# Kernel tuning notes

Hardware: AMD Instinct MI355X
Metric: run time of the kernel (lower is better)

The kernel has to match this reference:

```python
import jax, jax.numpy as jnp
import numpy as np

N = 100000
E = 1600000
F_IN = 128
F_OUT = 128


def setup_inputs() -> dict:
    key = jax.random.key(0)
    k1, k2, k3, k4 = jax.random.split(key, 4)
    x = jax.random.normal(k1, (N, F_IN), dtype=jnp.float32)
    edge_index = jax.random.randint(k2, (2, E), 0, N, dtype=jnp.int64)
    # GCNConv params (glorot weight, zero bias as in PyG defaults)
    limit = float(np.sqrt(6.0 / (F_IN + F_OUT)))
    W = jax.random.uniform(k3, (F_IN, F_OUT), minval=-limit, maxval=limit, dtype=jnp.float32)
    b = jnp.zeros((F_OUT,), dtype=jnp.float32)
    return {"x": x, "edge_index": edge_index, "W": W, "b": b}


def reference(x, edge_index, W, b):
    n = x.shape[0]
    # add self-loops
    loops = jnp.arange(n, dtype=edge_index.dtype)
    src = jnp.concatenate([edge_index[0], loops])  # source nodes j
    dst = jnp.concatenate([edge_index[1], loops])  # target nodes i
    # symmetric normalization: deg over incoming edges (targets), weight 1
    deg = jax.ops.segment_sum(jnp.ones_like(dst, dtype=x.dtype), dst, num_segments=n)
    dinv = jnp.where(deg > 0, jax.lax.rsqrt(deg), 0.0)
    norm = dinv[src] * dinv[dst]  # [E+N]
    # linear transform then message passing
    h = x @ W  # [N, F_OUT]
    msgs = h[src] * norm[:, None]  # gather + scale, [E+N, F_OUT]
    out = jax.ops.segment_sum(msgs, dst, num_segments=n)  # scatter-add
    return out + b
```

## Files before the change

kernel.cpp:

```cpp
#include <hip/hip_runtime.h>

#define FDIM 128
#define NBMAX 512
#define EPB 4096
#define CPAD 16

typedef __attribute__((ext_vector_type(8))) short bf16x8;
typedef __attribute__((ext_vector_type(4))) float f32x4;

__device__ __forceinline__ unsigned short f2bf(float f) {
    unsigned int u = __float_as_uint(f);
    unsigned int r = u + 0x7fffu + ((u >> 16) & 1u);
    return (unsigned short)(r >> 16);
}

__global__ __launch_bounds__(256) void k_prep(const int* __restrict__ dst,
                                              int* __restrict__ bcnt,
                                              const float* __restrict__ W,
                                              unsigned short* __restrict__ whi,
                                              int e, int ebl) {
    __shared__ int h[NBMAX];
    if ((int)blockIdx.x < ebl) {
        for (int i = threadIdx.x; i < NBMAX; i += 256) h[i] = 0;
        __syncthreads();
        int base = blockIdx.x * EPB;
        int end = min(base + EPB, e);
        for (int i = base + threadIdx.x; i < end; i += 256) atomicAdd(&h[dst[i] >> 8], 1);
        __syncthreads();
        for (int i = threadIdx.x; i < NBMAX; i += 256) {
            int c = h[i];
            if (c) atomicAdd(&bcnt[i * CPAD], c);
        }
    } else {
        int id = ((int)blockIdx.x - ebl) * 256 + threadIdx.x;
        int k = id >> 7, nn = id & 127;
        whi[nn * FDIM + k] = f2bf(W[id]);
    }
}

__global__ __launch_bounds__(256) void k_main(
    const int* __restrict__ src, const int* __restrict__ dst,
    const int* __restrict__ bcnt,
    int* __restrict__ gcur,
    unsigned int* __restrict__ coarse,
    const float* __restrict__ x, const unsigned short* __restrict__ whi,
    unsigned short* __restrict__ hs, int e, int n, int ebl) {
    union ShU {
        unsigned short Bs[FDIM * FDIM];
        struct {
            int sval[EPB];
            unsigned short sbkt[EPB];
            int loff[NBMAX];
            int gbs[NBMAX];
        } sc;
    };
    __shared__ ShU S;
    __shared__ int cur[NBMAX];
    __shared__ int bb[NBMAX];

    if ((int)blockIdx.x < ebl) {
        const int t = threadIdx.x;
        int* scr = S.sc.sval;

        int v0 = bcnt[t * CPAD], v1 = bcnt[(t + 256) * CPAD];
        scr[t] = v0;
        scr[t + 256] = v1;
        __syncthreads();
        for (int off = 1; off < NBMAX; off <<= 1) {
            int a0 = (t >= off) ? scr[t - off] : 0;
            int a1 = (t + 256 >= off) ? scr[t + 256 - off] : 0;
            __syncthreads();
            scr[t] += a0;
            scr[t + 256] += a1;
            __syncthreads();
        }
        bb[t] = scr[t] - v0;
        bb[t + 256] = scr[t + 256] - v1;

        cur[t] = 0;
        cur[t + 256] = 0;
        __syncthreads();
        int base = blockIdx.x * EPB;
        int end = min(base + EPB, e);
        int cnt = end - base;
        for (int i = base + t; i < end; i += 256) atomicAdd(&cur[dst[i] >> 8], 1);
        __syncthreads();

        int c0 = cur[t], c1 = cur[t + 256];
        scr[t] = c0;
        scr[t + 256] = c1;
        __syncthreads();
        for (int off = 1; off < NBMAX; off <<= 1) {
            int a0 = (t >= off) ? scr[t - off] : 0;
            int a1 = (t + 256 >= off) ? scr[t + 256 - off] : 0;
            __syncthreads();
            scr[t] += a0;
            scr[t + 256] += a1;
            __syncthreads();
        }
        S.sc.loff[t] = scr[t] - c0;
        S.sc.loff[t + 256] = scr[t + 256] - c1;
        S.sc.gbs[t] = bb[t] + (c0 ? atomicAdd(&gcur[t * CPAD], c0) : 0);
        S.sc.gbs[t + 256] = bb[t + 256] + (c1 ? atomicAdd(&gcur[(t + 256) * CPAD], c1) : 0);
        cur[t] = 0;
        cur[t + 256] = 0;
        __syncthreads();

        for (int i = base + t; i < end; i += 256) {
            int d = dst[i];
            int b = d >> 8;
            int lp = atomicAdd(&cur[b], 1);
            int pos = S.sc.loff[b] + lp;
            S.sc.sval[pos] = (int)(((unsigned)src[i] << 8) | (unsigned)(d & 255));
            S.sc.sbkt[pos] = (unsigned short)b;
        }
        __syncthreads();

        for (int s = t; s < cnt; s += 256) {
            int b = S.sc.sbkt[s];
            coarse[S.sc.gbs[b] + (s - S.sc.loff[b])] = (unsigned)S.sc.sval[s];
        }
    } else {
        {
            const float4* g4 = (const float4*)whi;
            float4* l4 = (float4*)S.Bs;
            for (int i = threadIdx.x; i < 2048; i += 256) {
                int nn = i >> 4;
                int g = i & 15;
                l4[nn * 16 + (g ^ (nn & 15))] = g4[i];
            }
        }
        __syncthreads();

        const int lane = threadIdx.x & 63;
        const int wid = threadIdx.x >> 6;
        const int m = lane & 15;
        const int quad = lane >> 4;
        const int row0 = ((int)blockIdx.x - ebl) * 64 + wid * 16;

        int rowA = row0 + m;
        if (rowA >= n) rowA = n - 1;
        const float* xr = x + (size_t)rowA * FDIM;

        f32x4 acc[8];
        #pragma unroll
        for (int ct = 0; ct < 8; ++ct) acc[ct] = (f32x4){0.f, 0.f, 0.f, 0.f};

        #pragma unroll
        for (int kc = 0; kc < 4; ++kc) {
            const int kb = kc * 32 + quad * 8;
            float4 xa = *(const float4*)(xr + kb);
            float4 xb = *(const float4*)(xr + kb + 4);
            float v[8] = {xa.x, xa.y, xa.z, xa.w, xb.x, xb.y, xb.z, xb.w};
            bf16x8 ahi, alo;
            #pragma unroll
            for (int j = 0; j < 8; ++j) {
                unsigned short hh = f2bf(v[j]);
                ahi[j] = (short)hh;
                alo[j] = (short)f2bf(v[j] - __uint_as_float(((unsigned)hh) << 16));
            }
            const int g = kc * 4 + quad;
            #pragma unroll
            for (int ct = 0; ct < 8; ++ct) {
                int nidx = ct * 16 + m;
                const bf16x8 bhi = *(const bf16x8*)(S.Bs + (size_t)nidx * FDIM + (g ^ m) * 8);
                acc[ct] = __builtin_amdgcn_mfma_f32_16x16x32_bf16(ahi, bhi, acc[ct], 0, 0, 0);
                acc[ct] = __builtin_amdgcn_mfma_f32_16x16x32_bf16(alo, bhi, acc[ct], 0, 0, 0);
            }
        }

        #pragma unroll
        for (int r = 0; r < 4; ++r) {
            int row = row0 + quad * 4 + r;
            if (row >= n) continue;
            unsigned short* hrow = hs + (size_t)row * FDIM;
            #pragma unroll
            for (int ct = 0; ct < 8; ++ct) hrow[ct * 16 + m] = f2bf(acc[ct][r]);
        }
    }
}

__global__ __launch_bounds__(256) void k_bfin(const unsigned int* __restrict__ coarse,
                                              const int* __restrict__ bcnt,
                                              float* __restrict__ dinv,
                                              int* __restrict__ row_start,
                                              int* __restrict__ ebuf, int n, int e) {
    __shared__ int bsc[NBMAX];
    __shared__ int ld[256];
    __shared__ int sc[256];
    __shared__ int cur[256];
    int b = blockIdx.x;
    int tt = threadIdx.x;
    bsc[tt] = bcnt[tt * CPAD];
    bsc[tt + 256] = bcnt[(tt + 256) * CPAD];
    __syncthreads();
    for (int off = 1; off < NBMAX; off <<= 1) {
        int a0 = (tt >= off) ? bsc[tt - off] : 0;
        int a1 = (tt + 256 >= off) ? bsc[tt + 256 - off] : 0;
        __syncthreads();
        bsc[tt] += a0;
        bsc[tt + 256] += a1;
        __syncthreads();
    }
    int s = (b > 0) ? bsc[b - 1] : 0;
    int t = bsc[b];
    if (b == 0 && tt == 0) row_start[n] = e;

    ld[tt] = 0;
    __syncthreads();
    for (int i = s + tt; i < t; i += 256) atomicAdd(&ld[coarse[i] & 255u], 1);
    __syncthreads();
    int v = ld[tt];
    sc[tt] = v;
    __syncthreads();
    for (int off = 1; off < 256; off <<= 1) {
        int tv = (tt >= off) ? sc[tt - off] : 0;
        __syncthreads();
        sc[tt] += tv;
        __syncthreads();
    }
    int rs = s + sc[tt] - v;
    cur[tt] = rs;
    int node = b * 256 + tt;
    if (node < n) {
        dinv[node] = rsqrtf((float)(v + 1));
        row_start[node] = rs;
    }
    __syncthreads();
    for (int i = s + tt; i < t; i += 256) {
        unsigned int p = coarse[i];
        int pos = atomicAdd(&cur[p & 255u], 1);
        ebuf[pos] = (int)(p >> 8);
    }
}

__global__ __launch_bounds__(256, 8) void k_gather(
    const unsigned short* __restrict__ hs, const int* __restrict__ ebuf,
    const int* __restrict__ row_start, const float* __restrict__ dinv,
    const float* __restrict__ bias, float* __restrict__ out, int n) {
    const int lane = threadIdx.x & 63;
    const int gw = (int)blockIdx.x * 4 + (threadIdx.x >> 6);
    const int nw = (int)gridDim.x * 4;

    const unsigned int* __restrict__ hl = (const unsigned int*)hs + lane;
    const float2 bb = ((const float2*)bias)[lane];

    for (int i = gw; i < n; i += nw) {
        int beg = row_start[i];
        int end = row_start[i + 1];
        float di = dinv[i];

        unsigned int u = hl[(unsigned)i << 6];
        float ax = di * __uint_as_float(u << 16);
        float ay = di * __uint_as_float(u & 0xffff0000u);
        float bx = 0.f, by = 0.f;

        int j = beg;
        int stop8 = j + ((end - j) & ~7);
        if (j < stop8) {
            int s0 = ebuf[j + 0], s1 = ebuf[j + 1], s2 = ebuf[j + 2], s3 = ebuf[j + 3];
            int s4 = ebuf[j + 4], s5 = ebuf[j + 5], s6 = ebuf[j + 6], s7 = ebuf[j + 7];
            j += 8;
            while (j < stop8) {
                unsigned int u0 = hl[(unsigned)s0 << 6], u1 = hl[(unsigned)s1 << 6];
                unsigned int u2 = hl[(unsigned)s2 << 6], u3 = hl[(unsigned)s3 << 6];
                unsigned int u4 = hl[(unsigned)s4 << 6], u5 = hl[(unsigned)s5 << 6];
                unsigned int u6 = hl[(unsigned)s6 << 6], u7 = hl[(unsigned)s7 << 6];
                float d0 = dinv[s0], d1 = dinv[s1], d2 = dinv[s2], d3 = dinv[s3];
                float d4 = dinv[s4], d5 = dinv[s5], d6 = dinv[s6], d7 = dinv[s7];
                int t0 = ebuf[j + 0], t1 = ebuf[j + 1], t2 = ebuf[j + 2], t3 = ebuf[j + 3];
                int t4 = ebuf[j + 4], t5 = ebuf[j + 5], t6 = ebuf[j + 6], t7 = ebuf[j + 7];
                ax = fmaf(d0, __uint_as_float(u0 << 16), ax);
                ay = fmaf(d0, __uint_as_float(u0 & 0xffff0000u), ay);
                bx = fmaf(d1, __uint_as_float(u1 << 16), bx);
                by = fmaf(d1, __uint_as_float(u1 & 0xffff0000u), by);
                ax = fmaf(d2, __uint_as_float(u2 << 16), ax);
                ay = fmaf(d2, __uint_as_float(u2 & 0xffff0000u), ay);
                bx = fmaf(d3, __uint_as_float(u3 << 16), bx);
                by = fmaf(d3, __uint_as_float(u3 & 0xffff0000u), by);
                ax = fmaf(d4, __uint_as_float(u4 << 16), ax);
                ay = fmaf(d4, __uint_as_float(u4 & 0xffff0000u), ay);
                bx = fmaf(d5, __uint_as_float(u5 << 16), bx);
                by = fmaf(d5, __uint_as_float(u5 & 0xffff0000u), by);
                ax = fmaf(d6, __uint_as_float(u6 << 16), ax);
                ay = fmaf(d6, __uint_as_float(u6 & 0xffff0000u), ay);
                bx = fmaf(d7, __uint_as_float(u7 << 16), bx);
                by = fmaf(d7, __uint_as_float(u7 & 0xffff0000u), by);
                s0 = t0; s1 = t1; s2 = t2; s3 = t3;
                s4 = t4; s5 = t5; s6 = t6; s7 = t7;
                j += 8;
            }
            {
                unsigned int u0 = hl[(unsigned)s0 << 6], u1 = hl[(unsigned)s1 << 6];
                unsigned int u2 = hl[(unsigned)s2 << 6], u3 = hl[(unsigned)s3 << 6];
                unsigned int u4 = hl[(unsigned)s4 << 6], u5 = hl[(unsigned)s5 << 6];
                unsigned int u6 = hl[(unsigned)s6 << 6], u7 = hl[(unsigned)s7 << 6];
                float d0 = dinv[s0], d1 = dinv[s1], d2 = dinv[s2], d3 = dinv[s3];
                float d4 = dinv[s4], d5 = dinv[s5], d6 = dinv[s6], d7 = dinv[s7];
                ax = fmaf(d0, __uint_as_float(u0 << 16), ax);
                ay = fmaf(d0, __uint_as_float(u0 & 0xffff0000u), ay);
                bx = fmaf(d1, __uint_as_float(u1 << 16), bx);
                by = fmaf(d1, __uint_as_float(u1 & 0xffff0000u), by);
                ax = fmaf(d2, __uint_as_float(u2 << 16), ax);
                ay = fmaf(d2, __uint_as_float(u2 & 0xffff0000u), ay);
                bx = fmaf(d3, __uint_as_float(u3 << 16), bx);
                by = fmaf(d3, __uint_as_float(u3 & 0xffff0000u), by);
                ax = fmaf(d4, __uint_as_float(u4 << 16), ax);
                ay = fmaf(d4, __uint_as_float(u4 & 0xffff0000u), ay);
                bx = fmaf(d5, __uint_as_float(u5 << 16), bx);
                by = fmaf(d5, __uint_as_float(u5 & 0xffff0000u), by);
                ax = fmaf(d6, __uint_as_float(u6 << 16), ax);
                ay = fmaf(d6, __uint_as_float(u6 & 0xffff0000u), ay);
                bx = fmaf(d7, __uint_as_float(u7 << 16), bx);
                by = fmaf(d7, __uint_as_float(u7 & 0xffff0000u), by);
            }
        }
        for (; j + 3 < end; j += 4) {
            int s0 = ebuf[j], s1 = ebuf[j + 1], s2 = ebuf[j + 2], s3 = ebuf[j + 3];
            float d0 = dinv[s0], d1 = dinv[s1], d2 = dinv[s2], d3 = dinv[s3];
            unsigned int u0 = hl[(unsigned)s0 << 6];
            unsigned int u1 = hl[(unsigned)s1 << 6];
            unsigned int u2 = hl[(unsigned)s2 << 6];
            unsigned int u3 = hl[(unsigned)s3 << 6];
            ax = fmaf(d0, __uint_as_float(u0 << 16), ax);
            ay = fmaf(d0, __uint_as_float(u0 & 0xffff0000u), ay);
            bx = fmaf(d1, __uint_as_float(u1 << 16), bx);
            by = fmaf(d1, __uint_as_float(u1 & 0xffff0000u), by);
            ax = fmaf(d2, __uint_as_float(u2 << 16), ax);
            ay = fmaf(d2, __uint_as_float(u2 & 0xffff0000u), ay);
            bx = fmaf(d3, __uint_as_float(u3 << 16), bx);
            by = fmaf(d3, __uint_as_float(u3 & 0xffff0000u), by);
        }
        for (; j < end; ++j) {
            int s0 = ebuf[j];
            float d0 = dinv[s0];
            unsigned int u0 = hl[(unsigned)s0 << 6];
            ax = fmaf(d0, __uint_as_float(u0 << 16), ax);
            ay = fmaf(d0, __uint_as_float(u0 & 0xffff0000u), ay);
        }
        ax += bx;
        ay += by;

        float2 r = make_float2(fmaf(ax, di, bb.x), fmaf(ay, di, bb.y));
        ((float2*)(out + (size_t)i * FDIM))[lane] = r;
    }
}

extern "C" void kernel_launch(void* const* d_in, const int* in_sizes, int n_in,
                              void* d_out, int out_size, void* d_ws, size_t ws_size,
                              hipStream_t stream) {
    const float* x  = (const float*)d_in[0];
    const int*   ei = (const int*)d_in[1];
    const float* W  = (const float*)d_in[2];
    const float* b  = (const float*)d_in[3];

    const int n = in_sizes[0] / FDIM;
    const int e = in_sizes[1] / 2;
    const int* src = ei;
    const int* dst = ei + e;
    float* out = (float*)d_out;

    const int nb = (n + 255) >> 8;
    const int ebl = (e + EPB - 1) / EPB;
    const int gemmbl = (n + 63) / 64;

    char* ws = (char*)d_ws;
    size_t off = 0;
    auto alloc = [&](size_t bytes) {
        char* p = ws + off;
        off += (bytes + 511) & ~(size_t)511;
        return p;
    };
    float*          dinv      = (float*)alloc((size_t)n * 4);
    int*            row_start = (int*)alloc((size_t)(n + 1) * 4);
    int*            bcnt      = (int*)alloc((size_t)NBMAX * CPAD * 4);
    int*            gcur      = (int*)alloc((size_t)NBMAX * CPAD * 4);
    unsigned short* whi       = (unsigned short*)alloc((size_t)FDIM * FDIM * 2);
    unsigned int*   coarse    = (unsigned int*)alloc((size_t)e * 4);
    int*            ebuf      = (int*)alloc((size_t)e * 4);
    unsigned short* hs        = (unsigned short*)alloc((size_t)n * FDIM * 2);

    hipMemsetAsync(bcnt, 0, (size_t)NBMAX * CPAD * 4 * 2, stream);

    k_prep<<<ebl + 64, 256, 0, stream>>>(dst, bcnt, W, whi, e, ebl);
    k_main<<<ebl + gemmbl, 256, 0, stream>>>(src, dst, bcnt, gcur, coarse, x, whi, hs, e, n, ebl);
    k_bfin<<<nb, 256, 0, stream>>>(coarse, bcnt, dinv, row_start, ebuf, n, e);
    {
        int blocks = (n + 3) / 4;
        if (blocks > 2048) blocks = 2048;
        k_gather<<<blocks, 256, 0, stream>>>(hs, ebuf, row_start, dinv, b, out, n);
    }
}
```

Baseline: 232.7 us.

## Fuse prep, sort and bucket-finalize into one cooperative persistent kernel with GEMM tickets

Replaces the three launches for counting, coarse bucketing plus GEMM, and per-bucket finalize with one cooperative kernel of 512 persistent blocks separated by grid.sync. Blocks that have no sort chunk take GEMM tiles from an atomic ticket counter before the second sync. All blocks drain the remaining tiles after the finalize phase, so the GEMM overlaps with the sort and finalize work. This is meant to remove launch gaps and tail idle time, at the cost of grid-wide barriers. It also caps occupancy at 512 resident blocks.

After: 357.9 us. 53.8% more time.

```diff
diff --git a/kernel.cpp b/kernel.cpp
--- a/kernel.cpp
+++ b/kernel.cpp
@@ -1,9 +1,14 @@
 #include <hip/hip_runtime.h>
+#include <hip/hip_cooperative_groups.h>
+
+namespace cg = cooperative_groups;
 
 #define FDIM 128
 #define NBMAX 512
 #define EPB 4096
 #define CPAD 16
+#define NBLK 512
+#define B1 6
 
 typedef __attribute__((ext_vector_type(8))) short bf16x8;
 typedef __attribute__((ext_vector_type(4))) float f32x4;
@@ -14,37 +19,75 @@
     return (unsigned short)(r >> 16);
 }
 
-__global__ __launch_bounds__(256) void k_prep(const int* __restrict__ dst,
-                                              int* __restrict__ bcnt,
-                                              const float* __restrict__ W,
-                                              unsigned short* __restrict__ whi,
-                                              int e, int ebl) {
-    __shared__ int h[NBMAX];
-    if ((int)blockIdx.x < ebl) {
-        for (int i = threadIdx.x; i < NBMAX; i += 256) h[i] = 0;
-        __syncthreads();
-        int base = blockIdx.x * EPB;
-        int end = min(base + EPB, e);
-        for (int i = base + threadIdx.x; i < end; i += 256) atomicAdd(&h[dst[i] >> 8], 1);
-        __syncthreads();
-        for (int i = threadIdx.x; i < NBMAX; i += 256) {
-            int c = h[i];
-            if (c) atomicAdd(&bcnt[i * CPAD], c);
-        }
-    } else {
-        int id = ((int)blockIdx.x - ebl) * 256 + threadIdx.x;
-        int k = id >> 7, nn = id & 127;
-        whi[nn * FDIM + k] = f2bf(W[id]);
-    }
-}
-
-__global__ __launch_bounds__(256) void k_main(
+__device__ __forceinline__ void gemm_tile(int tt, const float* __restrict__ x,
+                                          const unsigned short* Bs,
+                                          unsigned short* __restrict__ hs, int n, int tid) {
+    const int lane = tid & 63;
+    const int wid = tid >> 6;
+    const int m = lane & 15;
+    const int quad = lane >> 4;
+    const int row0 = tt * 64 + wid * 16;
+
+    int rowA = row0 + m;
+    if (rowA >= n) rowA = n - 1;
+    const float* xr = x + (size_t)rowA * FDIM;
+
+    f32x4 acc[8];
+    #pragma unroll
+    for (int ct = 0; ct < 8; ++ct) acc[ct] = (f32x4){0.f, 0.f, 0.f, 0.f};
+
+    #pragma unroll
+    for (int kc = 0; kc < 4; ++kc) {
+        const int kb = kc * 32 + quad * 8;
+        float4 xa = *(const float4*)(xr + kb);
+        float4 xb = *(const float4*)(xr + kb + 4);
+        float v[8] = {xa.x, xa.y, xa.z, xa.w, xb.x, xb.y, xb.z, xb.w};
+        bf16x8 ahi, alo;
+        #pragma unroll
+        for (int j = 0; j < 8; ++j) {
+            unsigned short hh = f2bf(v[j]);
+            ahi[j] = (short)hh;
+            alo[j] = (short)f2bf(v[j] - __uint_as_float(((unsigned)hh) << 16));
+        }
+        const int g = kc * 4 + quad;
+        #pragma unroll
+        for (int ct = 0; ct < 8; ++ct) {
+            int nidx = ct * 16 + m;
+            const bf16x8 bhi = *(const bf16x8*)(Bs + (size_t)nidx * FDIM + (g ^ m) * 8);
+            acc[ct] = __builtin_amdgcn_mfma_f32_16x16x32_bf16(ahi, bhi, acc[ct], 0, 0, 0);
+            acc[ct] = __builtin_amdgcn_mfma_f32_16x16x32_bf16(alo, bhi, acc[ct], 0, 0, 0);
+        }
+    }
+
+    #pragma unroll
+    for (int r = 0; r < 4; ++r) {
+        int row = row0 + quad * 4 + r;
+        if (row >= n) continue;
+        unsigned short* hrow = hs + (size_t)row * FDIM;
+        #pragma unroll
+        for (int ct = 0; ct < 8; ++ct) hrow[ct * 16 + m] = f2bf(acc[ct][r]);
+    }
+}
+
+__device__ __forceinline__ void stage_Bs(const unsigned short* __restrict__ whi,
+                                         unsigned short* Bs, int tid) {
+    const float4* g4 = (const float4*)whi;
+    float4* l4 = (float4*)Bs;
+    for (int i = tid; i < 2048; i += 256) {
+        int nn = i >> 4;
+        int g = i & 15;
+        l4[nn * 16 + (g ^ (nn & 15))] = g4[i];
+    }
+}
+
+__global__ __launch_bounds__(256, 2) void k_fused(
     const int* __restrict__ src, const int* __restrict__ dst,
-    const int* __restrict__ bcnt,
-    int* __restrict__ gcur,
+    int* __restrict__ bcnt, int* __restrict__ gcur, int* __restrict__ gtick,
     unsigned int* __restrict__ coarse,
-    const float* __restrict__ x, const unsigned short* __restrict__ whi,
-    unsigned short* __restrict__ hs, int e, int n, int ebl) {
+    const float* __restrict__ x, const float* __restrict__ W,
+    unsigned short* __restrict__ whi, unsigned short* __restrict__ hs,
+    float* __restrict__ dinv, int* __restrict__ row_start, int* __restrict__ ebuf,
+    int e, int n, int nchunks, int nb, int ntiles) {
     union ShU {
         unsigned short Bs[FDIM * FDIM];
         struct {
@@ -53,184 +96,165 @@
             int loff[NBMAX];
             int gbs[NBMAX];
         } sc;
+        struct { int ld[256]; int pf[256]; int pos[256]; } bf;
     };
     __shared__ ShU S;
     __shared__ int cur[NBMAX];
-    __shared__ int bb[NBMAX];
-
-    if ((int)blockIdx.x < ebl) {
-        const int t = threadIdx.x;
+    __shared__ int bb[NBMAX + 1];
+    __shared__ int tkt;
+
+    const int bid = (int)blockIdx.x;
+    const int tid = (int)threadIdx.x;
+    cg::grid_group grid = cg::this_grid();
+
+    for (int c = bid; c < nchunks; c += NBLK) {
+        cur[tid] = 0;
+        cur[tid + 256] = 0;
+        __syncthreads();
+        int base = c * EPB, end2 = min(base + EPB, e);
+        for (int i = base + tid; i < end2; i += 256) atomicAdd(&cur[dst[i] >> 8], 1);
+        __syncthreads();
+        for (int i = tid; i < NBMAX; i += 256) {
+            int cc = cur[i];
+            if (cc) atomicAdd(&bcnt[i * CPAD], cc);
+        }
+        __syncthreads();
+    }
+    for (int id = bid * 256 + tid; id < FDIM * FDIM; id += NBLK * 256) {
+        int k = id >> 7, nn = id & 127;
+        whi[nn * FDIM + k] = f2bf(W[id]);
+    }
+
+    grid.sync();
+
+    {
         int* scr = S.sc.sval;
-
-        int v0 = bcnt[t * CPAD], v1 = bcnt[(t + 256) * CPAD];
-        scr[t] = v0;
-        scr[t + 256] = v1;
+        int v0 = bcnt[tid * CPAD], v1 = bcnt[(tid + 256) * CPAD];
+        scr[tid] = v0;
+        scr[tid + 256] = v1;
         __syncthreads();
         for (int off = 1; off < NBMAX; off <<= 1) {
-            int a0 = (t >= off) ? scr[t - off] : 0;
-            int a1 = (t + 256 >= off) ? scr[t + 256 - off] : 0;
-            __syncthreads();
-            scr[t] += a0;
-            scr[t + 256] += a1;
-            __syncthreads();
-        }
-        bb[t] = scr[t] - v0;
-        bb[t + 256] = scr[t + 256] - v1;
-
-        cur[t] = 0;
-        cur[t + 256] = 0;
-        __syncthreads();
-        int base = blockIdx.x * EPB;
-        int end = min(base + EPB, e);
-        int cnt = end - base;
-        for (int i = base + t; i < end; i += 256) atomicAdd(&cur[dst[i] >> 8], 1);
-        __syncthreads();
-
-        int c0 = cur[t], c1 = cur[t + 256];
-        scr[t] = c0;
-        scr[t + 256] = c1;
-        __syncthreads();
-        for (int off = 1; off < NBMAX; off <<= 1) {
-            int a0 = (t >= off) ? scr[t - off] : 0;
-            int a1 = (t + 256 >= off) ? scr[t + 256 - off] : 0;
-            __syncthreads();
-            scr[t] += a0;
-            scr[t + 256] += a1;
-            __syncthreads();
-        }
-        S.sc.loff[t] = scr[t] - c0;
-        S.sc.loff[t + 256] = scr[t + 256] - c1;
-        S.sc.gbs[t] = bb[t] + (c0 ? atomicAdd(&gcur[t * CPAD], c0) : 0);
-        S.sc.gbs[t + 256] = bb[t + 256] + (c1 ? atomicAdd(&gcur[(t + 256) * CPAD], c1) : 0);
-        cur[t] = 0;
-        cur[t + 256] = 0;
-        __syncthreads();
-
-        for (int i = base + t; i < end; i += 256) {
-            int d = dst[i];
-            int b = d >> 8;
-            int lp = atomicAdd(&cur[b], 1);
-            int pos = S.sc.loff[b] + lp;
-            S.sc.sval[pos] = (int)(((unsigned)src[i] << 8) | (unsigned)(d & 255));
-            S.sc.sbkt[pos] = (unsigned short)b;
-        }
-        __syncthreads();
-
-        for (int s = t; s < cnt; s += 256) {
-            int b = S.sc.sbkt[s];
-            coarse[S.sc.gbs[b] + (s - S.sc.loff[b])] = (unsigned)S.sc.sval[s];
+            int a0 = (tid >= off) ? scr[tid - off] : 0;
+            int a1 = (tid + 256 >= off) ? scr[tid + 256 - off] : 0;
+            __syncthreads();
+            scr[tid] += a0;
+            scr[tid + 256] += a1;
+            __syncthreads();
+        }
+        bb[tid] = scr[tid] - v0;
+        bb[tid + 256] = scr[tid + 256] - v1;
+        if (tid == 0) bb[NBMAX] = e;
+        __syncthreads();
+    }
+
+    bool staged = false;
+
+    if (bid < nchunks) {
+        for (int c = bid; c < nchunks; c += NBLK) {
+            int* scr = S.sc.sval;
+            cur[tid] = 0;
+            cur[tid + 256] = 0;
+            __syncthreads();
+            int base = c * EPB, end2 = min(base + EPB, e), cnt = end2 - base;
+            for (int i = base + tid; i < end2; i += 256) atomicAdd(&cur[dst[i] >> 8], 1);
+            __syncthreads();
+            int c0 = cur[tid], c1 = cur[tid + 256];
+            scr[tid] = c0;
+            scr[tid + 256] = c1;
+            __syncthreads();
+            for (int off = 1; off < NBMAX; off <<= 1) {
+                int a0 = (tid >= off) ? scr[tid - off] : 0;
+                int a1 = (tid + 256 >= off) ? scr[tid + 256 - off] : 0;
+                __syncthreads();
+                scr[tid] += a0;
+                scr[tid + 256] += a1;
+                __syncthreads();
+            }
+            S.sc.loff[tid] = scr[tid] - c0;
+            S.sc.loff[tid + 256] = scr[tid + 256] - c1;
+            S.sc.gbs[tid] = bb[tid] + (c0 ? atomicAdd(&gcur[tid * CPAD], c0) : 0);
+            S.sc.gbs[tid + 256] = bb[tid + 256] + (c1 ? atomicAdd(&gcur[(tid + 256) * CPAD], c1) : 0);
+            cur[tid] = 0;
+            cur[tid + 256] = 0;
+            __syncthreads();
+            for (int i = base + tid; i < end2; i += 256) {
+                int d = dst[i];
+                int b = d >> 8;
+                int lp = atomicAdd(&cur[b], 1);
+                int p2 = S.sc.loff[b] + lp;
+                S.sc.sval[p2] = (int)(((unsigned)src[i] << 8) | (unsigned)(d & 255));
+                S.sc.sbkt[p2] = (unsigned short)b;
+            }
+            __syncthreads();
+            for (int s2 = tid; s2 < cnt; s2 += 256) {
+                int b = S.sc.sbkt[s2];
+                coarse[S.sc.gbs[b] + (s2 - S.sc.loff[b])] = (unsigned)S.sc.sval[s2];
+            }
+            __syncthreads();
         }
     } else {
-        {
-            const float4* g4 = (const float4*)whi;
-            float4* l4 = (float4*)S.Bs;
-            for (int i = threadIdx.x; i < 2048; i += 256) {
-                int nn = i >> 4;
-                int g = i & 15;
-                l4[nn * 16 + (g ^ (nn & 15))] = g4[i];
-            }
-        }
-        __syncthreads();
-
-        const int lane = threadIdx.x & 63;
-        const int wid = threadIdx.x >> 6;
-        const int m = lane & 15;
-        const int quad = lane >> 4;
-        const int row0 = ((int)blockIdx.x - ebl) * 64 + wid * 16;
-
-        int rowA = row0 + m;
-        if (rowA >= n) rowA = n - 1;
-        const float* xr = x + (size_t)rowA * FDIM;
-
-        f32x4 acc[8];
-        #pragma unroll
-        for (int ct = 0; ct < 8; ++ct) acc[ct] = (f32x4){0.f, 0.f, 0.f, 0.f};
-
-        #pragma unroll
-        for (int kc = 0; kc < 4; ++kc) {
-            const int kb = kc * 32 + quad * 8;
-            float4 xa = *(const float4*)(xr + kb);
-            float4 xb = *(const float4*)(xr + kb + 4);
-            float v[8] = {xa.x, xa.y, xa.z, xa.w, xb.x, xb.y, xb.z, xb.w};
-            bf16x8 ahi, alo;
-            #pragma unroll
-            for (int j = 0; j < 8; ++j) {
-                unsigned short hh = f2bf(v[j]);
-                ahi[j] = (short)hh;
-                alo[j] = (short)f2bf(v[j] - __uint_as_float(((unsigned)hh) << 16));
-            }
-            const int g = kc * 4 + quad;
-            #pragma unroll
-            for (int ct = 0; ct < 8; ++ct) {
-                int nidx = ct * 16 + m;
-                const bf16x8 bhi = *(const bf16x8*)(S.Bs + (size_t)nidx * FDIM + (g ^ m) * 8);
-                acc[ct] = __builtin_amdgcn_mfma_f32_16x16x32_bf16(ahi, bhi, acc[ct], 0, 0, 0);
-                acc[ct] = __builtin_amdgcn_mfma_f32_16x16x32_bf16(alo, bhi, acc[ct], 0, 0, 0);
-            }
-        }
-
-        #pragma unroll
-        for (int r = 0; r < 4; ++r) {
-            int row = row0 + quad * 4 + r;
-            if (row >= n) continue;
-            unsigned short* hrow = hs + (size_t)row * FDIM;
-            #pragma unroll
-            for (int ct = 0; ct < 8; ++ct) hrow[ct * 16 + m] = f2bf(acc[ct][r]);
-        }
-    }
-}
-
-__global__ __launch_bounds__(256) void k_bfin(const unsigned int* __restrict__ coarse,
-                                              const int* __restrict__ bcnt,
-                                              float* __restrict__ dinv,
-                                              int* __restrict__ row_start,
-                                              int* __restrict__ ebuf, int n, int e) {
-    __shared__ int bsc[NBMAX];
-    __shared__ int ld[256];
-    __shared__ int sc[256];
-    __shared__ int cur[256];
-    int b = blockIdx.x;
-    int tt = threadIdx.x;
-    bsc[tt] = bcnt[tt * CPAD];
-    bsc[tt + 256] = bcnt[(tt + 256) * CPAD];
-    __syncthreads();
-    for (int off = 1; off < NBMAX; off <<= 1) {
-        int a0 = (tt >= off) ? bsc[tt - off] : 0;
-        int a1 = (tt + 256 >= off) ? bsc[tt + 256 - off] : 0;
-        __syncthreads();
-        bsc[tt] += a0;
-        bsc[tt + 256] += a1;
-        __syncthreads();
-    }
-    int s = (b > 0) ? bsc[b - 1] : 0;
-    int t = bsc[b];
-    if (b == 0 && tt == 0) row_start[n] = e;
-
-    ld[tt] = 0;
-    __syncthreads();
-    for (int i = s + tt; i < t; i += 256) atomicAdd(&ld[coarse[i] & 255u], 1);
-    __syncthreads();
-    int v = ld[tt];
-    sc[tt] = v;
-    __syncthreads();
-    for (int off = 1; off < 256; off <<= 1) {
-        int tv = (tt >= off) ? sc[tt - off] : 0;
-        __syncthreads();
-        sc[tt] += tv;
-        __syncthreads();
-    }
-    int rs = s + sc[tt] - v;
-    cur[tt] = rs;
-    int node = b * 256 + tt;
-    if (node < n) {
-        dinv[node] = rsqrtf((float)(v + 1));
-        row_start[node] = rs;
-    }
-    __syncthreads();
-    for (int i = s + tt; i < t; i += 256) {
-        unsigned int p = coarse[i];
-        int pos = atomicAdd(&cur[p & 255u], 1);
-        ebuf[pos] = (int)(p >> 8);
+        for (int k = 0; k < B1; ++k) {
+            __syncthreads();
+            if (tid == 0) tkt = atomicAdd(gtick, 1);
+            __syncthreads();
+            int t = tkt;
+            if (t >= ntiles) break;
+            if (!staged) {
+                stage_Bs(whi, S.Bs, tid);
+                staged = true;
+                __syncthreads();
+            }
+            gemm_tile(t, x, S.Bs, hs, n, tid);
+        }
+    }
+
+    grid.sync();
+
+    for (int b2 = bid; b2 < nb; b2 += NBLK) {
+        int s = bb[b2], t = bb[b2 + 1];
+        __syncthreads();
+        S.bf.ld[tid] = 0;
+        __syncthreads();
+        for (int i = s + tid; i < t; i += 256) atomicAdd(&S.bf.ld[coarse[i] & 255u], 1);
+        __syncthreads();
+        int v = S.bf.ld[tid];
+        S.bf.pf[tid] = v;
+        __syncthreads();
+        for (int off = 1; off < 256; off <<= 1) {
+            int tv = (tid >= off) ? S.bf.pf[tid - off] : 0;
+            __syncthreads();
+            S.bf.pf[tid] += tv;
+            __syncthreads();
+        }
+        int rs = s + S.bf.pf[tid] - v;
+        S.bf.pos[tid] = rs;
+        int node = b2 * 256 + tid;
+        if (node < n) {
+            dinv[node] = rsqrtf((float)(v + 1));
+            row_start[node] = rs;
+        }
+        __syncthreads();
+        for (int i = s + tid; i < t; i += 256) {
+            unsigned int p = coarse[i];
+            int pp = atomicAdd(&S.bf.pos[p & 255u], 1);
+            ebuf[pp] = (int)(p >> 8);
+        }
+        __syncthreads();
+    }
+    if (bid == 0 && tid == 0) row_start[n] = e;
+
+    while (true) {
+        __syncthreads();
+        if (tid == 0) tkt = atomicAdd(gtick, 1);
+        __syncthreads();
+        int t = tkt;
+        if (t >= ntiles) break;
+        if (!staged) {
+            stage_Bs(whi, S.Bs, tid);
+            staged = true;
+            __syncthreads();
+        }
+        gemm_tile(t, x, S.Bs, hs, n, tid);
     }
 }
 
@@ -354,15 +378,15 @@
     const float* W  = (const float*)d_in[2];
     const float* b  = (const float*)d_in[3];
 
-    const int n = in_sizes[0] / FDIM;
-    const int e = in_sizes[1] / 2;
+    int n = in_sizes[0] / FDIM;
+    int e = in_sizes[1] / 2;
     const int* src = ei;
     const int* dst = ei + e;
     float* out = (float*)d_out;
 
-    const int nb = (n + 255) >> 8;
-    const int ebl = (e + EPB - 1) / EPB;
-    const int gemmbl = (n + 63) / 64;
+    int nb = (n + 255) >> 8;
+    int nchunks = (e + EPB - 1) / EPB;
+    int ntiles = (n + 63) / 64;
 
     char* ws = (char*)d_ws;
     size_t off = 0;
@@ -375,16 +399,22 @@
     int*            row_start = (int*)alloc((size_t)(n + 1) * 4);
     int*            bcnt      = (int*)alloc((size_t)NBMAX * CPAD * 4);
     int*            gcur      = (int*)alloc((size_t)NBMAX * CPAD * 4);
+    int*            gtick     = (int*)alloc(512);
     unsigned short* whi       = (unsigned short*)alloc((size_t)FDIM * FDIM * 2);
     unsigned int*   coarse    = (unsigned int*)alloc((size_t)e * 4);
     int*            ebuf      = (int*)alloc((size_t)e * 4);
     unsigned short* hs        = (unsigned short*)alloc((size_t)n * FDIM * 2);
 
-    hipMemsetAsync(bcnt, 0, (size_t)NBMAX * CPAD * 4 * 2, stream);
-
-    k_prep<<<ebl + 64, 256, 0, stream>>>(dst, bcnt, W, whi, e, ebl);
-    k_main<<<ebl + gemmbl, 256, 0, stream>>>(src, dst, bcnt, gcur, coarse, x, whi, hs, e, n, ebl);
-    k_bfin<<<nb, 256, 0, stream>>>(coarse, bcnt, dinv, row_start, ebuf, n, e);
+    hipMemsetAsync(bcnt, 0, (size_t)NBMAX * CPAD * 4 * 2 + 512, stream);
+
+    {
+        void* args[] = {
+            (void*)&src, (void*)&dst, (void*)&bcnt, (void*)&gcur, (void*)&gtick,
+            (void*)&coarse, (void*)&x, (void*)&W, (void*)&whi, (void*)&hs,
+            (void*)&dinv, (void*)&row_start, (void*)&ebuf,
+            (void*)&e, (void*)&n, (void*)&nchunks, (void*)&nb, (void*)&ntiles};
+        hipLaunchCooperativeKernel((const void*)k_fused, dim3(NBLK), dim3(256), args, 0, stream);
+    }
     {
         int blocks = (n + 3) / 4;
         if (blocks > 2048) blocks = 2048;
```
